# Optimization experiments

Measured on AMD Instinct MI355X. Metric: run time of the kernel, lower is better.

## Reference

```python
import jax, jax.numpy as jnp
import numpy as np

RADIUS = 1.0
N_NORM = 1  # default n_norm in the torch module


def setup_inputs() -> dict:
    key = jax.random.key(0)
    k1, k2, k3 = jax.random.split(key, 3)
    batch, n, c_in, c_out = 8, 2048, 64, 64
    features = jax.random.normal(k1, (batch, n, c_in), dtype=jnp.float32)
    geometry = jax.random.normal(k2, (batch, n, 3), dtype=jnp.float32)
    # learned per-edge kernel weight: K(diff)[o,i] = sum_x diff[x] * Wk[x,o,i]
    Wk = jax.random.normal(k3, (3, c_out, c_in), dtype=jnp.float32) * 0.1
    return {"features": features, "geometry": geometry, "Wk": Wk}


def reference(features, geometry, Wk):
    # diff[z,a,b,:] = geometry[z,b] - geometry[z,a]   (rb - ra in the torch code)
    diff = geometry[:, None, :, :] - geometry[:, :, None, :]  # [z, a, b, 3]
    norm = jnp.sqrt(jnp.sum(diff * diff, axis=-1))            # [z, a, b]
    # Dense masked formulation: padding every point's neighbor list to k = n
    # with rel_mask zeros is mathematically identical to the torch variable-k
    # padding (masked entries contribute nothing to the einsum reduce).
    rel_mask = (norm < RADIUS).astype(features.dtype)         # [z, a, b]
    # Fused reduce. Original: einsum('zab,zabij,zabj->zai', mask, K(diff), feat[nei])
    # with K(diff)[z,a,b,i,j] = einsum('zabx,xij->zabij', diff, Wk). We contract
    # over b first to avoid materializing the [z,a,b,i,j] kernel tensor.
    s = jnp.einsum('zab,zabx,zbj->zaxj', rel_mask, diff, features)  # [z, a, 3, c_in]
    out = jnp.einsum('zaxj,xij->zai', s, Wk) / jnp.sqrt(jnp.asarray(N_NORM, features.dtype))
    return out
```

## Files before the change

kernel.cpp:

```cpp
#include <hip/hip_runtime.h>
#include <stdint.h>

#define NPTS 2048

#define BP_OFF    0ULL
#define BP_BYTES  (8ULL * 16 * 64 * 1024)
#define W2F_OFF   (BP_OFF + BP_BYTES)
#define W2F_BYTES (24ULL * 1024)
#define WXF_OFF   (W2F_OFF + W2F_BYTES)
#define WXF_BYTES (24ULL * 1024)
#define MW_OFF    (WXF_OFF + WXF_BYTES)
#define MW_BYTES  (8ULL * 32 * 64 * 256)

typedef __attribute__((ext_vector_type(8))) short bf16x8;
typedef __attribute__((ext_vector_type(4))) float f32x4;
typedef __attribute__((ext_vector_type(4))) unsigned int u32x4;

__device__ __forceinline__ unsigned f2bf(float f) {
  union { float f; unsigned u; } v; v.f = f;
  return (v.u + 0x7FFFu + ((v.u >> 16) & 1u)) >> 16;
}

__device__ __forceinline__ bf16x8 pack8(const float4 a, const float4 b) {
  u32x4 r;
  r[0] = f2bf(a.x) | (f2bf(a.y) << 16);
  r[1] = f2bf(a.z) | (f2bf(a.w) << 16);
  r[2] = f2bf(b.x) | (f2bf(b.y) << 16);
  r[3] = f2bf(b.z) | (f2bf(b.w) << 16);
  union { u32x4 u; bf16x8 h; } c; c.u = r; return c.h;
}

__device__ __forceinline__ bf16x8 unpack_mask(unsigned mq) {
  const unsigned dep0 = ((mq & 15u) * 0x204081u) & 0x01010101u;
  const unsigned dep1 = (((mq >> 4) & 15u) * 0x204081u) & 0x01010101u;
  u32x4 aw;
  aw[0] = __builtin_amdgcn_perm(dep0, 0u, 0x0C050C04u) * 0x3F80u;
  aw[1] = __builtin_amdgcn_perm(dep0, 0u, 0x0C070C06u) * 0x3F80u;
  aw[2] = __builtin_amdgcn_perm(dep1, 0u, 0x0C050C04u) * 0x3F80u;
  aw[3] = __builtin_amdgcn_perm(dep1, 0u, 0x0C070C06u) * 0x3F80u;
  union { u32x4 u; bf16x8 h; } cv; cv.u = aw;
  return cv.h;
}

__global__ __launch_bounds__(256, 2) void k1_prep(const float* __restrict__ feat,
                                                  const float* __restrict__ geom,
                                                  const float* __restrict__ Wk,
                                                  unsigned char* __restrict__ ws) {
  const int blk = blockIdx.x, t = threadIdx.x;
  if (blk < 512) {
    const int z = blk >> 6, s = blk & 63;
    __shared__ float FT[64][37];
    __shared__ float g[96];
    __shared__ float gxp[2048], gyp[2048], gzp[2048];
    const float* fz = feat + ((size_t)z * NPTS + s * 32) * 64;
    const float* gz = geom + (size_t)z * NPTS * 3;
    {
      const int row = t >> 3, j0 = (t & 7) << 3;
      const float4 v0 = *(const float4*)&fz[row * 64 + j0];
      const float4 v1 = *(const float4*)&fz[row * 64 + j0 + 4];
      FT[j0 + 0][row] = v0.x; FT[j0 + 1][row] = v0.y;
      FT[j0 + 2][row] = v0.z; FT[j0 + 3][row] = v0.w;
      FT[j0 + 4][row] = v1.x; FT[j0 + 5][row] = v1.y;
      FT[j0 + 6][row] = v1.z; FT[j0 + 7][row] = v1.w;
    }
    if (t < 96) g[t] = gz[s * 96 + t];
    {
      float v[24];
#pragma unroll
      for (int i = 0; i < 6; ++i) *(float4*)&v[i * 4] = *(const float4*)&gz[t * 24 + i * 4];
#pragma unroll
      for (int i = 0; i < 8; ++i) {
        const int pp = i * 256 + t;
        gxp[pp] = v[i * 3 + 0]; gyp[pp] = v[i * 3 + 1]; gzp[pp] = v[i * 3 + 2];
      }
    }
    __syncthreads();

    {
      const int w = t >> 6, L = t & 63;
      const int nn = L >> 2, k0 = (L & 3) * 8;
      const int j = w * 16 + nn;
      float f[8];
#pragma unroll
      for (int i = 0; i < 8; ++i) f[i] = FT[j][k0 + i];
      float gx[3][8];
#pragma unroll
      for (int x = 0; x < 3; ++x)
#pragma unroll
        for (int i = 0; i < 8; ++i) gx[x][i] = g[(k0 + i) * 3 + x];
      unsigned char* base = ws + BP_OFF + (size_t)z * 1048576 + (size_t)w * 65536 +
                            (size_t)s * 1024 + L * 16;
#pragma unroll
      for (int it = 0; it < 4; ++it) {
        u32x4 pv;
#pragma unroll
        for (int p = 0; p < 4; ++p) {
          float f0 = f[2 * p], f1 = f[2 * p + 1];
          if (it < 3) { f0 *= gx[it][2 * p]; f1 *= gx[it][2 * p + 1]; }
          pv[p] = f2bf(f0) | (f2bf(f1) << 16);
        }
        *(u32x4*)(base + (size_t)it * 4 * 65536) = pv;
      }
    }

    {
      float ax[8], ay[8], az[8];
#pragma unroll
      for (int i = 0; i < 8; ++i) {
        const int pp = i * 256 + t;
        ax[i] = gxp[pp]; ay[i] = gyp[pp]; az[i] = gzp[pp];
      }
      unsigned bits[8] = {0, 0, 0, 0, 0, 0, 0, 0};
      for (int j = 0; j < 32; ++j) {
        const float bx = g[j * 3 + 0], by = g[j * 3 + 1], bz = g[j * 3 + 2];
#pragma unroll
        for (int i = 0; i < 8; ++i) {
          const float d0 = bx - ax[i], d1 = by - ay[i], d2 = bz - az[i];
          const float n2 = fmaf(d2, d2, fmaf(d1, d1, d0 * d0));
          bits[i] |= (n2 < 1.0f ? 1u : 0u) << j;
        }
      }
      unsigned int* mw = (unsigned int*)(ws + MW_OFF);
#pragma unroll
      for (int i = 0; i < 8; ++i) {
        const int r = t * 8 + i;
        mw[(((size_t)z * 32 + (r >> 6)) * 64 + s) * 64 + (r & 15) * 4 + ((r >> 4) & 3)] = bits[i];
      }
    }
  } else if (blk == 512) {
    for (int e = t; e < 1536; e += 256) {
      const int frag = e >> 6, lp = e & 63, nn = lp >> 2, qd = lp & 3;
      const int kb = frag >> 2, cb = frag & 3;
      u32x4 pv;
#pragma unroll
      for (int p = 0; p < 4; ++p) {
        const int k0 = kb * 32 + qd * 8 + 2 * p;
        const float v0 = Wk[(k0 >> 6) * 4096 + (cb * 16 + nn) * 64 + (k0 & 63)];
        const float v1 = Wk[((k0 + 1) >> 6) * 4096 + (cb * 16 + nn) * 64 + ((k0 + 1) & 63)];
        pv[p] = f2bf(v0) | (f2bf(v1) << 16);
      }
      *(u32x4*)(ws + W2F_OFF + (size_t)frag * 1024 + lp * 16) = pv;
    }
  } else {
    for (int e = t; e < 1536; e += 256) {
      const int frag = e >> 6, lp = e & 63, nn = lp >> 2, qd = lp & 3;
      const int kb = frag / 12, cb = frag % 12, xi = cb * 16 + nn;
      u32x4 pv;
#pragma unroll
      for (int p = 0; p < 4; ++p) {
        const int k0 = kb * 32 + qd * 8 + 2 * p;
        const float v0 = Wk[(xi >> 6) * 4096 + (xi & 63) * 64 + k0];
        const float v1 = Wk[(xi >> 6) * 4096 + (xi & 63) * 64 + k0 + 1];
        pv[p] = f2bf(v0) | (f2bf(v1) << 16);
      }
      *(u32x4*)(ws + WXF_OFF + (size_t)frag * 1024 + lp * 16) = pv;
    }
  }
}

__global__ __launch_bounds__(512, 2) void k2_gemm(const float* __restrict__ geom,
                                                  const unsigned char* __restrict__ ws,
                                                  float* __restrict__ out) {
  __shared__ __align__(16) float Ct[64 * 256];

  const int t = threadIdx.x, lane = t & 63, w = t >> 6;
  const int quad = (lane >> 4) & 3, n = lane & 15;
  const int bx = blockIdx.x;
  const int z = bx & 7, at = bx >> 3, a0 = at * 64;
  const int fragoff = n * 64 + quad * 16;
  const int qsh = quad * 8;

  const unsigned char* bpz = ws + BP_OFF + (size_t)z * 1048576 + (size_t)(2 * w) * 65536;
  const unsigned char* mwz = ws + MW_OFF + ((size_t)z * 32 + at) * 16384;

  f32x4 acc[4][2];
#pragma unroll
  for (int rg = 0; rg < 4; ++rg)
#pragma unroll
    for (int cb = 0; cb < 2; ++cb)
#pragma unroll
      for (int r = 0; r < 4; ++r) acc[rg][cb][r] = 0.f;

  bf16x8 Bf[4][2];
  u32x4 Mf[4];
#pragma unroll
  for (int sl = 0; sl < 4; ++sl) {
#pragma unroll
    for (int cb = 0; cb < 2; ++cb)
      Bf[sl][cb] = *(const bf16x8*)(bpz + (size_t)cb * 65536 + (size_t)sl * 1024 + fragoff);
    Mf[sl] = *(const u32x4*)(mwz + sl * 256 + n * 16);
  }

#define KSTEP(S, SL)                                                           \
  {                                                                            \
    const u32x4 mw = Mf[SL];                                                   \
    _Pragma("unroll") for (int rg = 0; rg < 4; ++rg) {                         \
      const bf16x8 Af = unpack_mask((mw[rg] >> qsh) & 0xFFu);                  \
      _Pragma("unroll") for (int cb = 0; cb < 2; ++cb)                         \
        acc[rg][cb] = __builtin_amdgcn_mfma_f32_16x16x32_bf16(                 \
            Af, Bf[SL][cb], acc[rg][cb], 0, 0, 0);                             \
    }                                                                          \
    const int sp = (S) + 4 > 63 ? 63 : (S) + 4;                                \
    Mf[SL] = *(const u32x4*)(mwz + sp * 256 + n * 16);                         \
    _Pragma("unroll") for (int cb = 0; cb < 2; ++cb)                           \
      Bf[SL][cb] = *(const bf16x8*)(bpz + (size_t)cb * 65536 +                 \
                                    (size_t)sp * 1024 + fragoff);              \
  }

  for (int s4 = 0; s4 < 64; s4 += 4) {
    KSTEP(s4 + 0, 0) KSTEP(s4 + 1, 1) KSTEP(s4 + 2, 2) KSTEP(s4 + 3, 3)
  }
#undef KSTEP

#pragma unroll
  for (int rg = 0; rg < 4; ++rg)
#pragma unroll
    for (int cb = 0; cb < 2; ++cb)
#pragma unroll
      for (int r = 0; r < 4; ++r) {
        const int row = rg * 16 + quad * 4 + r;
        const int col = 32 * w + cb * 16 + n;
        Ct[row * 256 + (((col >> 2) ^ row) << 2) + (col & 3)] = acc[rg][cb][r];
      }
  __syncthreads();

  if (w < 4) {
    const int lm = 16 * w + n;
    bf16x8 Across[8];
#pragma unroll
    for (int kb = 0; kb < 8; ++kb) {
      const int c0 = (kb * 8 + quad * 2) ^ lm;
      const int c1 = (kb * 8 + quad * 2 + 1) ^ lm;
      const float4 f0 = *(const float4*)&Ct[lm * 256 + c0 * 4];
      const float4 f1 = *(const float4*)&Ct[lm * 256 + c1 * 4];
      Across[kb] = pack8(f0, f1);
    }

    f32x4 mn[4], V[12];
#pragma unroll
    for (int i = 0; i < 4; ++i)
#pragma unroll
      for (int r = 0; r < 4; ++r) mn[i][r] = 0.f;
#pragma unroll
    for (int i = 0; i < 12; ++i)
#pragma unroll
      for (int r = 0; r < 4; ++r) V[i][r] = 0.f;

    const unsigned char* w2f = ws + W2F_OFF;
    const unsigned char* wxf = ws + WXF_OFF;
#pragma unroll
    for (int kb = 0; kb < 6; ++kb)
#pragma unroll
      for (int cb = 0; cb < 4; ++cb) {
        const bf16x8 Bfr = *(const bf16x8*)(w2f + (size_t)(kb * 4 + cb) * 1024 + fragoff);
        mn[cb] = __builtin_amdgcn_mfma_f32_16x16x32_bf16(Across[kb], Bfr, mn[cb], 0, 0, 0);
      }
#pragma unroll
    for (int kb = 0; kb < 2; ++kb)
#pragma unroll
      for (int cb = 0; cb < 12; ++cb) {
        const bf16x8 Bfr = *(const bf16x8*)(wxf + (size_t)(kb * 12 + cb) * 1024 + fragoff);
        V[cb] = __builtin_amdgcn_mfma_f32_16x16x32_bf16(Across[6 + kb], Bfr, V[cb], 0, 0, 0);
      }

#pragma unroll
    for (int r = 0; r < 4; ++r) {
      const int af = a0 + 16 * w + quad * 4 + r;
      const float g0 = geom[((size_t)z * NPTS + af) * 3 + 0];
      const float g1 = geom[((size_t)z * NPTS + af) * 3 + 1];
      const float g2 = geom[((size_t)z * NPTS + af) * 3 + 2];
#pragma unroll
      for (int cb = 0; cb < 4; ++cb) {
        const float v = mn[cb][r] - g0 * V[cb][r] - g1 * V[cb + 4][r] - g2 * V[cb + 8][r];
        out[((size_t)z * NPTS + af) * 64 + cb * 16 + n] = v;
      }
    }
  }
}

extern "C" void kernel_launch(void* const* d_in, const int* in_sizes, int n_in,
                              void* d_out, int out_size, void* d_ws, size_t ws_size,
                              hipStream_t stream) {
  const float* feat = (const float*)d_in[0];
  const float* geom = (const float*)d_in[1];
  const float* Wk   = (const float*)d_in[2];
  float* out = (float*)d_out;
  unsigned char* ws = (unsigned char*)d_ws;

  k1_prep<<<dim3(514), 256, 0, stream>>>(feat, geom, Wk, ws);
  k2_gemm<<<dim3(256), 512, 0, stream>>>(geom, ws, out);
}
```

Baseline: 103.2 us.

## Switch main mask GEMM to 32x32x16 MFMA with matching B-fragment layout

Replaces the 16x16x32 bf16 MFMA tiles in the masked reduction GEMM with 32x32x16 MFMA instructions. The B-operand pre-pack in the first kernel is relaid out to fit the new fragment shape. Mask words are loaded as scalar dwords per lane and unpacked into four A fragments per k-step. The goal is fewer MFMA issues and fewer mask unpacks per k-step, at the cost of new index math that must match exactly across the producer and consumer kernels.

```diff
diff --git a/kernel.cpp b/kernel.cpp
--- a/kernel.cpp
+++ b/kernel.cpp
@@ -4,7 +4,7 @@
 #define NPTS 2048
 
 #define BP_OFF    0ULL
-#define BP_BYTES  (8ULL * 16 * 64 * 1024)
+#define BP_BYTES  (8ULL * 8 * 64 * 2 * 1024)
 #define W2F_OFF   (BP_OFF + BP_BYTES)
 #define W2F_BYTES (24ULL * 1024)
 #define WXF_OFF   (W2F_OFF + W2F_BYTES)
@@ -14,6 +14,7 @@
 
 typedef __attribute__((ext_vector_type(8))) short bf16x8;
 typedef __attribute__((ext_vector_type(4))) float f32x4;
+typedef __attribute__((ext_vector_type(16))) float f32x16;
 typedef __attribute__((ext_vector_type(4))) unsigned int u32x4;
 
 __device__ __forceinline__ unsigned f2bf(float f) {
@@ -88,8 +89,10 @@
       for (int x = 0; x < 3; ++x)
 #pragma unroll
         for (int i = 0; i < 8; ++i) gx[x][i] = g[(k0 + i) * 3 + x];
-      unsigned char* base = ws + BP_OFF + (size_t)z * 1048576 + (size_t)w * 65536 +
-                            (size_t)s * 1024 + L * 16;
+      const int kc = (L & 3) >> 1, h = (L & 3) & 1;
+      const int lane16 = h * 32 + (w & 1) * 16 + nn;
+      unsigned char* base = ws + BP_OFF + (size_t)z * 1048576 + (size_t)(w >> 1) * 131072 +
+                            (size_t)s * 2048 + (size_t)kc * 1024 + (size_t)lane16 * 16;
 #pragma unroll
       for (int it = 0; it < 4; ++it) {
         u32x4 pv;
@@ -99,7 +102,7 @@
           if (it < 3) { f0 *= gx[it][2 * p]; f1 *= gx[it][2 * p + 1]; }
           pv[p] = f2bf(f0) | (f2bf(f1) << 16);
         }
-        *(u32x4*)(base + (size_t)it * 4 * 65536) = pv;
+        *(u32x4*)(base + (size_t)it * 262144) = pv;
       }
     }
 
@@ -164,47 +167,47 @@
   __shared__ __align__(16) float Ct[64 * 256];
 
   const int t = threadIdx.x, lane = t & 63, w = t >> 6;
+  const int l31 = lane & 31;
+  const int h8 = (lane >> 5) << 3;
   const int quad = (lane >> 4) & 3, n = lane & 15;
+  const int fragoff = n * 64 + quad * 16;
   const int bx = blockIdx.x;
   const int z = bx & 7, at = bx >> 3, a0 = at * 64;
-  const int fragoff = n * 64 + quad * 16;
-  const int qsh = quad * 8;
-
-  const unsigned char* bpz = ws + BP_OFF + (size_t)z * 1048576 + (size_t)(2 * w) * 65536;
+
+  const unsigned char* bpz = ws + BP_OFF + (size_t)z * 1048576 + (size_t)w * 131072;
   const unsigned char* mwz = ws + MW_OFF + ((size_t)z * 32 + at) * 16384;
-
-  f32x4 acc[4][2];
-#pragma unroll
-  for (int rg = 0; rg < 4; ++rg)
-#pragma unroll
-    for (int cb = 0; cb < 2; ++cb)
-#pragma unroll
-      for (int r = 0; r < 4; ++r) acc[rg][cb][r] = 0.f;
+  const int midx = ((l31 & 15) * 4 + (l31 >> 4)) * 4;
+
+  f32x16 acc0, acc1;
+#pragma unroll
+  for (int r = 0; r < 16; ++r) { acc0[r] = 0.f; acc1[r] = 0.f; }
 
   bf16x8 Bf[4][2];
-  u32x4 Mf[4];
+  unsigned Mf0[4], Mf1[4];
 #pragma unroll
   for (int sl = 0; sl < 4; ++sl) {
-#pragma unroll
-    for (int cb = 0; cb < 2; ++cb)
-      Bf[sl][cb] = *(const bf16x8*)(bpz + (size_t)cb * 65536 + (size_t)sl * 1024 + fragoff);
-    Mf[sl] = *(const u32x4*)(mwz + sl * 256 + n * 16);
+    Bf[sl][0] = *(const bf16x8*)(bpz + (size_t)sl * 2048 + (size_t)lane * 16);
+    Bf[sl][1] = *(const bf16x8*)(bpz + (size_t)sl * 2048 + 1024 + (size_t)lane * 16);
+    Mf0[sl] = *(const unsigned*)(mwz + sl * 256 + midx);
+    Mf1[sl] = *(const unsigned*)(mwz + sl * 256 + midx + 8);
   }
 
 #define KSTEP(S, SL)                                                           \
   {                                                                            \
-    const u32x4 mw = Mf[SL];                                                   \
-    _Pragma("unroll") for (int rg = 0; rg < 4; ++rg) {                         \
-      const bf16x8 Af = unpack_mask((mw[rg] >> qsh) & 0xFFu);                  \
-      _Pragma("unroll") for (int cb = 0; cb < 2; ++cb)                         \
-        acc[rg][cb] = __builtin_amdgcn_mfma_f32_16x16x32_bf16(                 \
-            Af, Bf[SL][cb], acc[rg][cb], 0, 0, 0);                             \
-    }                                                                          \
+    const unsigned m0 = Mf0[SL], m1 = Mf1[SL];                                 \
+    const bf16x8 A00 = unpack_mask((m0 >> h8) & 0xFFu);                        \
+    const bf16x8 A10 = unpack_mask((m1 >> h8) & 0xFFu);                        \
+    const bf16x8 A01 = unpack_mask((m0 >> (16 + h8)) & 0xFFu);                 \
+    const bf16x8 A11 = unpack_mask((m1 >> (16 + h8)) & 0xFFu);                 \
+    acc0 = __builtin_amdgcn_mfma_f32_32x32x16_bf16(A00, Bf[SL][0], acc0, 0, 0, 0); \
+    acc1 = __builtin_amdgcn_mfma_f32_32x32x16_bf16(A10, Bf[SL][0], acc1, 0, 0, 0); \
+    acc0 = __builtin_amdgcn_mfma_f32_32x32x16_bf16(A01, Bf[SL][1], acc0, 0, 0, 0); \
+    acc1 = __builtin_amdgcn_mfma_f32_32x32x16_bf16(A11, Bf[SL][1], acc1, 0, 0, 0); \
     const int sp = (S) + 4 > 63 ? 63 : (S) + 4;                                \
-    Mf[SL] = *(const u32x4*)(mwz + sp * 256 + n * 16);                         \
-    _Pragma("unroll") for (int cb = 0; cb < 2; ++cb)                           \
-      Bf[SL][cb] = *(const bf16x8*)(bpz + (size_t)cb * 65536 +                 \
-                                    (size_t)sp * 1024 + fragoff);              \
+    Mf0[SL] = *(const unsigned*)(mwz + sp * 256 + midx);                       \
+    Mf1[SL] = *(const unsigned*)(mwz + sp * 256 + midx + 8);                   \
+    Bf[SL][0] = *(const bf16x8*)(bpz + (size_t)sp * 2048 + (size_t)lane * 16); \
+    Bf[SL][1] = *(const bf16x8*)(bpz + (size_t)sp * 2048 + 1024 + (size_t)lane * 16); \
   }
 
   for (int s4 = 0; s4 < 64; s4 += 4) {
@@ -212,16 +215,17 @@
   }
 #undef KSTEP
 
-#pragma unroll
-  for (int rg = 0; rg < 4; ++rg)
-#pragma unroll
-    for (int cb = 0; cb < 2; ++cb)
-#pragma unroll
-      for (int r = 0; r < 4; ++r) {
-        const int row = rg * 16 + quad * 4 + r;
-        const int col = 32 * w + cb * 16 + n;
-        Ct[row * 256 + (((col >> 2) ^ row) << 2) + (col & 3)] = acc[rg][cb][r];
-      }
+  {
+    const int rh = 4 * (lane >> 5);
+#pragma unroll
+    for (int r = 0; r < 16; ++r) {
+      const int row = (r & 3) + 8 * (r >> 2) + rh;
+      const int col = 32 * w + l31;
+      Ct[row * 256 + (((col >> 2) ^ row) << 2) + (col & 3)] = acc0[r];
+      const int row1 = row + 32;
+      Ct[row1 * 256 + (((col >> 2) ^ row1) << 2) + (col & 3)] = acc1[r];
+    }
+  }
   __syncthreads();
 
   if (w < 4) {
```

After: 103.1 us. About the same (-0.0%).
